# Kernel tuning notes

Measured on AMD Instinct MI355X. Metric: run time of the kernel, lower is better.

The kernel has to match this reference:

```python
import jax, jax.numpy as jnp
import numpy as np

N = 50000      # nodes
E = 800000     # edges
D_IN = 128
D_H = 128
D_OUT = 40
BN_EPS = 1e-5


def setup_inputs() -> dict:
    key = jax.random.key(0)
    ks = jax.random.split(key, 12)
    x = jax.random.normal(ks[0], (N, D_IN), dtype=jnp.float32)
    edge_index = jax.random.randint(ks[1], (2, E), 0, N, dtype=jnp.int32)
    s = 0.05
    W1 = jax.random.normal(ks[2], (D_IN, D_H), dtype=jnp.float32) * s
    b1 = jnp.zeros((D_H,), jnp.float32)
    W2 = jax.random.normal(ks[3], (D_H, D_H), dtype=jnp.float32) * s
    b2 = jnp.zeros((D_H,), jnp.float32)
    W3 = jax.random.normal(ks[4], (D_H, D_OUT), dtype=jnp.float32) * s
    b3 = jnp.zeros((D_OUT,), jnp.float32)
    # BatchNorm (eval mode: running stats)
    g1 = jnp.ones((D_H,), jnp.float32)
    be1 = jnp.zeros((D_H,), jnp.float32)
    m1 = jax.random.normal(ks[5], (D_H,), dtype=jnp.float32) * 0.1
    v1 = jax.random.uniform(ks[6], (D_H,), dtype=jnp.float32, minval=0.5, maxval=1.5)
    g2 = jnp.ones((D_H,), jnp.float32)
    be2 = jnp.zeros((D_H,), jnp.float32)
    m2 = jax.random.normal(ks[7], (D_H,), dtype=jnp.float32) * 0.1
    v2 = jax.random.uniform(ks[8], (D_H,), dtype=jnp.float32, minval=0.5, maxval=1.5)
    return {"x": x, "edge_index": edge_index,
            "W1": W1, "b1": b1, "W2": W2, "b2": b2, "W3": W3, "b3": b3,
            "g1": g1, "be1": be1, "m1": m1, "v1": v1,
            "g2": g2, "be2": be2, "m2": m2, "v2": v2}


def gcn_conv(x, W, b, src, dst):
    # PyG GCNConv: h = x W; A_hat = D^-1/2 (A + I) D^-1/2; out = A_hat h + b
    h = x @ W                                   # [N, d_out]
    deg = jnp.zeros((N,), h.dtype).at[dst].add(1.0) + 1.0   # degrees incl. self loop
    dis = jax.lax.rsqrt(deg)                    # deg^-1/2
    norm = dis[src] * dis[dst]                  # [E]
    msg = h[src] * norm[:, None]                # [E, d_out] gather + scale
    agg = jax.ops.segment_sum(msg, dst, num_segments=N)     # scatter-add
    agg = agg + h * (1.0 / deg)[:, None]        # self-loop term: dis_i*dis_i = 1/deg_i
    return agg + b


def bn_eval(x, gamma, beta, mean, var):
    return (x - mean) * jax.lax.rsqrt(var + BN_EPS) * gamma + beta


def reference(x, edge_index, W1, b1, W2, b2, W3, b3,
              g1, be1, m1, v1, g2, be2, m2, v2):
    src, dst = edge_index[0], edge_index[1]
    h = jax.nn.relu(bn_eval(gcn_conv(x, W1, b1, src, dst), g1, be1, m1, v1))
    h = jax.nn.relu(bn_eval(gcn_conv(h, W2, b2, src, dst), g2, be2, m2, v2))
    h = gcn_conv(h, W3, b3, src, dst)
    return jax.nn.log_softmax(h, axis=-1)
```

## Files before the change

### kernel.cpp

```cpp
#include <hip/hip_runtime.h>
#include <math.h>

#define BN_EPS 1e-5f

typedef __attribute__((ext_vector_type(8))) short bf16x8;
typedef __attribute__((ext_vector_type(4))) float f32x4;

__device__ inline unsigned f2bf(float f) {
  union { float f; unsigned u; } v; v.f = f;
  unsigned r = v.u + 0x7FFF + ((v.u >> 16) & 1);
  return r >> 16;
}

__device__ inline void acc8n(float* a, uint4 v) {
  a[0] += __uint_as_float(v.x << 16);
  a[1] += __uint_as_float(v.x & 0xffff0000u);
  a[2] += __uint_as_float(v.y << 16);
  a[3] += __uint_as_float(v.y & 0xffff0000u);
  a[4] += __uint_as_float(v.z << 16);
  a[5] += __uint_as_float(v.z & 0xffff0000u);
  a[6] += __uint_as_float(v.w << 16);
  a[7] += __uint_as_float(v.w & 0xffff0000u);
}

__device__ inline void acc4n(float* a, uint2 v) {
  a[0] += __uint_as_float(v.x << 16);
  a[1] += __uint_as_float(v.x & 0xffff0000u);
  a[2] += __uint_as_float(v.y << 16);
  a[3] += __uint_as_float(v.y & 0xffff0000u);
}


__global__ void k_zero(uint4* __restrict__ deg, int n16, uint4* __restrict__ flags) {
  int i = blockIdx.x * blockDim.x + threadIdx.x;
  if (i < n16) deg[i] = make_uint4(0, 0, 0, 0);
  if (i < 16) flags[i] = make_uint4(0, 0, 0, 0);
}


__global__ __launch_bounds__(256) void k_count_prep(
    const int* __restrict__ ei, int E, int* __restrict__ deg, int* __restrict__ posw,
    const float* __restrict__ W1, const float* __restrict__ W2,
    const float* __restrict__ W3,
    const float* __restrict__ g1, const float* __restrict__ be1,
    const float* __restrict__ m1, const float* __restrict__ v1,
    const float* __restrict__ g2, const float* __restrict__ be2,
    const float* __restrict__ m2, const float* __restrict__ v2,
    const float* __restrict__ b1, const float* __restrict__ b2,
    const float* __restrict__ b3,
    ushort* __restrict__ WT1, ushort* __restrict__ WT2, ushort* __restrict__ WT3,
    float* __restrict__ sc1, float* __restrict__ sh1,
    float* __restrict__ sc2, float* __restrict__ sh2,
    float* __restrict__ b3pad) {
  int b = blockIdx.x;
  int tid = threadIdx.x;
  if (b < 64) {
    int k = b * 2 + (tid >> 7);
    int n = tid & 127;
    WT1[n * 128 + k] = (ushort)f2bf(W1[k * 128 + n]);
    WT2[n * 128 + k] = (ushort)f2bf(W2[k * 128 + n]);
    WT3[n * 128 + k] = (n < 40) ? (ushort)f2bf(W3[k * 40 + n]) : (ushort)0;
    if (k == 0) {
      float s1 = g1[n] * rsqrtf(v1[n] + BN_EPS);
      sc1[n] = s1; sh1[n] = be1[n] + (b1[n] - m1[n]) * s1;
      float s2 = g2[n] * rsqrtf(v2[n] + BN_EPS);
      sc2[n] = s2; sh2[n] = be2[n] + (b2[n] - m2[n]) * s2;
    } else if (k == 1 && n < 64) {
      b3pad[n] = (n < 40) ? b3[n] : 0.f;
    }
    return;
  }
  int e = (b - 64) * 256 + tid;
  if (e < E) posw[e] = atomicAdd(&deg[ei[E + e]], 1);
}

__global__ void k_scan(const int* __restrict__ deg, int* __restrict__ rowstart,
                       float* __restrict__ dis, int* __restrict__ flags,
                       int n, int E) {
  __shared__ int s[1024];
  __shared__ int spre;
  const int b = blockIdx.x;
  const int tid = threadIdx.x;
  int i = b * 1024 + tid;
  int v = (i < n) ? deg[i] : 0;
  if (i < n) dis[i] = rsqrtf((float)(v + 1));
  s[tid] = v;
  __syncthreads();
  for (int off = 1; off < 1024; off <<= 1) {
    int t = (tid >= off) ? s[tid - off] : 0;
    __syncthreads();
    s[tid] += t;
    __syncthreads();
  }
  if (tid == 0) {
    spre = 0;
    atomicExch(&flags[b], s[1023] + 1);
  }
  __syncthreads();
  if (tid < b) {
    int v2;
    do { v2 = atomicAdd(&flags[tid], 0); } while (v2 == 0);
    atomicAdd(&spre, v2 - 1);
  }
  __syncthreads();
  int pre = spre;
  if (i < n) rowstart[i] = pre + s[tid] - v;
  if (b == 0 && tid == 0) rowstart[n] = E;
}


template <bool F32A, bool FILL>
__global__ __launch_bounds__(256) void k_gemm_bf16(const void* __restrict__ Ap,
                                                   const ushort* __restrict__ WT,
                                                   ushort* __restrict__ C,
                                                   const float* __restrict__ dis,
                                                   int nrows, int NC, int gemmBlocks,
                                                   const int* __restrict__ ei,
                                                   const int* __restrict__ rowstart,
                                                   const int* __restrict__ posw,
                                                   unsigned* __restrict__ slot, int E) {
  if (FILL && (int)blockIdx.x >= gemmBlocks) {
    int e = ((int)blockIdx.x - gemmBlocks) * 256 + threadIdx.x;
    if (e < E) slot[rowstart[ei[E + e]] + posw[e]] = (unsigned)ei[e];
    return;
  }
  __shared__ ushort As[64][80];
  __shared__ ushort Bs[128][80];
  const int tid  = threadIdx.x;
  const int lane = tid & 63;
  const int wid  = tid >> 6;
  const int wr   = wid >> 1, wc = wid & 1;
  const int row0 = blockIdx.x * 64;
  f32x4 acc[2][4] = {};

  const int mrow = lane & 15;
  const int kg   = (lane >> 4) * 8;

  for (int k0 = 0; k0 < 128; k0 += 64) {
    __syncthreads();
    for (int i = tid; i < 512; i += 256) {
      int r = i >> 3, c = (i & 7) * 8;
      uint4 w = make_uint4(0, 0, 0, 0);
      if (row0 + r < nrows) {
        if (F32A) {
          const float* A = (const float*)Ap;
          float4 v0 = *(const float4*)(A + (size_t)(row0 + r) * 128 + k0 + c);
          float4 v1 = *(const float4*)(A + (size_t)(row0 + r) * 128 + k0 + c + 4);
          w.x = f2bf(v0.x) | (f2bf(v0.y) << 16);
          w.y = f2bf(v0.z) | (f2bf(v0.w) << 16);
          w.z = f2bf(v1.x) | (f2bf(v1.y) << 16);
          w.w = f2bf(v1.z) | (f2bf(v1.w) << 16);
        } else {
          const ushort* A = (const ushort*)Ap;
          w = *(const uint4*)(A + (size_t)(row0 + r) * 128 + k0 + c);
        }
      }
      *(uint4*)(&As[r][c]) = w;
    }
    for (int i = tid; i < 1024; i += 256) {
      int r = i >> 3, c = (i & 7) * 8;
      *(uint4*)(&Bs[r][c]) = *(const uint4*)(WT + r * 128 + k0 + c);
    }
    __syncthreads();

#pragma unroll
    for (int ks = 0; ks < 2; ks++) {
      bf16x8 a[2], b[4];
#pragma unroll
      for (int f = 0; f < 2; f++)
        a[f] = *(const bf16x8*)(&As[wr * 32 + f * 16 + mrow][ks * 32 + kg]);
#pragma unroll
      for (int f = 0; f < 4; f++)
        b[f] = *(const bf16x8*)(&Bs[wc * 64 + f * 16 + mrow][ks * 32 + kg]);
#pragma unroll
      for (int fm = 0; fm < 2; fm++)
#pragma unroll
        for (int fn = 0; fn < 4; fn++)
          acc[fm][fn] = __builtin_amdgcn_mfma_f32_16x16x32_bf16(a[fm], b[fn], acc[fm][fn], 0, 0, 0);
    }
  }

  const int rl = (lane >> 4) * 4;
  const int cl = lane & 15;
#pragma unroll
  for (int fm = 0; fm < 2; fm++) {
#pragma unroll
    for (int r = 0; r < 4; r++) {
      int row = row0 + wr * 32 + fm * 16 + rl + r;
      if (row >= nrows) continue;
      float dn = dis[row];
#pragma unroll
      for (int fn = 0; fn < 4; fn++) {
        int col = wc * 64 + fn * 16 + cl;
        if (col < NC) C[(size_t)row * NC + col] = (ushort)f2bf(acc[fm][fn][r] * dn);
      }
    }
  }
}


__global__ __launch_bounds__(256) void k_agg128b(const ushort* __restrict__ h,
                          const int* __restrict__ rowstart,
                          const unsigned* __restrict__ slot,
                          const float* __restrict__ dis,
                          const float* __restrict__ bnsc,
                          const float* __restrict__ bnsh,
                          ushort* __restrict__ out, int nnodes) {
  int node = blockIdx.x * 4 + threadIdx.y;
  if (node >= nnodes) return;
  int lane = threadIdx.x;
  int eg = lane >> 4, cl = lane & 15, c0 = cl * 8;
  int s = rowstart[node], e = rowstart[node + 1];
  int deg = e - s;
  unsigned mys = 0;
  if (lane < deg) mys = slot[s + lane];
  float a[8] = {0.f, 0.f, 0.f, 0.f, 0.f, 0.f, 0.f, 0.f};
  int nb = deg < 64 ? deg : 64;
  int i = eg;
  for (; i + 12 < nb; i += 16) {
    int s0 = __shfl((int)mys, i);
    int s1 = __shfl((int)mys, i + 4);
    int s2 = __shfl((int)mys, i + 8);
    int s3 = __shfl((int)mys, i + 12);
    uint4 h0 = *(const uint4*)(h + (size_t)s0 * 128 + c0);
    uint4 h1 = *(const uint4*)(h + (size_t)s1 * 128 + c0);
    uint4 h2 = *(const uint4*)(h + (size_t)s2 * 128 + c0);
    uint4 h3 = *(const uint4*)(h + (size_t)s3 * 128 + c0);
    acc8n(a, h0); acc8n(a, h1); acc8n(a, h2); acc8n(a, h3);
  }
  for (; i + 4 < nb; i += 8) {
    int s0 = __shfl((int)mys, i);
    int s1 = __shfl((int)mys, i + 4);
    uint4 h0 = *(const uint4*)(h + (size_t)s0 * 128 + c0);
    uint4 h1 = *(const uint4*)(h + (size_t)s1 * 128 + c0);
    acc8n(a, h0); acc8n(a, h1);
  }
  if (i < nb) {
    int s0 = __shfl((int)mys, i);
    uint4 h0 = *(const uint4*)(h + (size_t)s0 * 128 + c0);
    acc8n(a, h0);
  }
  for (int j = s + 64 + eg; j < e; j += 4) {
    uint4 h0 = *(const uint4*)(h + (size_t)slot[j] * 128 + c0);
    acc8n(a, h0);
  }
#pragma unroll
  for (int j = 0; j < 8; j++) {
    a[j] += __shfl_xor(a[j], 16);
    a[j] += __shfl_xor(a[j], 32);
  }
  if (eg == 0) {
    uint4 hv = *(const uint4*)(h + (size_t)node * 128 + c0);
    acc8n(a, hv);
    float dn = dis[node];
    float4 sc0 = *(const float4*)(bnsc + c0), sc1 = *(const float4*)(bnsc + c0 + 4);
    float4 sh0 = *(const float4*)(bnsh + c0), sh1 = *(const float4*)(bnsh + c0 + 4);
    float o0 = fmaxf(fmaf(a[0] * dn, sc0.x, sh0.x), 0.f);
    float o1 = fmaxf(fmaf(a[1] * dn, sc0.y, sh0.y), 0.f);
    float o2 = fmaxf(fmaf(a[2] * dn, sc0.z, sh0.z), 0.f);
    float o3 = fmaxf(fmaf(a[3] * dn, sc0.w, sh0.w), 0.f);
    float o4 = fmaxf(fmaf(a[4] * dn, sc1.x, sh1.x), 0.f);
    float o5 = fmaxf(fmaf(a[5] * dn, sc1.y, sh1.y), 0.f);
    float o6 = fmaxf(fmaf(a[6] * dn, sc1.z, sh1.z), 0.f);
    float o7 = fmaxf(fmaf(a[7] * dn, sc1.w, sh1.w), 0.f);
    uint4 w;
    w.x = f2bf(o0) | (f2bf(o1) << 16);
    w.y = f2bf(o2) | (f2bf(o3) << 16);
    w.z = f2bf(o4) | (f2bf(o5) << 16);
    w.w = f2bf(o6) | (f2bf(o7) << 16);
    *(uint4*)(out + (size_t)node * 128 + c0) = w;
  }
}


__global__ __launch_bounds__(256) void k_agg40_lsm(const ushort* __restrict__ h,
                            const int* __restrict__ rowstart,
                            const unsigned* __restrict__ slot,
                            const float* __restrict__ dis,
                            const float* __restrict__ b3pad,
                            float* __restrict__ out, int nnodes) {
  int node = blockIdx.x * 4 + threadIdx.y;
  if (node >= nnodes) return;
  int lane = threadIdx.x;
  int eg = lane >> 4, cl = lane & 15, c0 = cl * 4;
  bool act = cl < 10;
  int s = rowstart[node], e = rowstart[node + 1];
  int deg = e - s;
  unsigned mys = 0;
  if (lane < deg) mys = slot[s + lane];
  float a[4] = {0.f, 0.f, 0.f, 0.f};
  int nb = deg < 64 ? deg : 64;
  int i = eg;
  for (; i + 12 < nb; i += 16) {
    int s0 = __shfl((int)mys, i);
    int s1 = __shfl((int)mys, i + 4);
    int s2 = __shfl((int)mys, i + 8);
    int s3 = __shfl((int)mys, i + 12);
    if (act) {
      uint2 h0 = *(const uint2*)(h + (size_t)s0 * 40 + c0);
      uint2 h1 = *(const uint2*)(h + (size_t)s1 * 40 + c0);
      uint2 h2 = *(const uint2*)(h + (size_t)s2 * 40 + c0);
      uint2 h3 = *(const uint2*)(h + (size_t)s3 * 40 + c0);
      acc4n(a, h0); acc4n(a, h1); acc4n(a, h2); acc4n(a, h3);
    }
  }
  for (; i + 4 < nb; i += 8) {
    int s0 = __shfl((int)mys, i);
    int s1 = __shfl((int)mys, i + 4);
    if (act) {
      uint2 h0 = *(const uint2*)(h + (size_t)s0 * 40 + c0);
      uint2 h1 = *(const uint2*)(h + (size_t)s1 * 40 + c0);
      acc4n(a, h0); acc4n(a, h1);
    }
  }
  if (i < nb) {
    int s0 = __shfl((int)mys, i);
    if (act) acc4n(a, *(const uint2*)(h + (size_t)s0 * 40 + c0));
  }
  for (int j = s + 64 + eg; j < e; j += 4) {
    unsigned sj = slot[j];
    if (act) acc4n(a, *(const uint2*)(h + (size_t)sj * 40 + c0));
  }
#pragma unroll
  for (int j = 0; j < 4; j++) {
    a[j] += __shfl_xor(a[j], 16);
    a[j] += __shfl_xor(a[j], 32);
  }
  if (act) {
    acc4n(a, *(const uint2*)(h + (size_t)node * 40 + c0));
    float dn = dis[node];
    float4 bb = *(const float4*)(b3pad + c0);
    a[0] = fmaf(a[0], dn, bb.x);
    a[1] = fmaf(a[1], dn, bb.y);
    a[2] = fmaf(a[2], dn, bb.z);
    a[3] = fmaf(a[3], dn, bb.w);
  }
  float m = act ? fmaxf(fmaxf(a[0], a[1]), fmaxf(a[2], a[3])) : -INFINITY;
#pragma unroll
  for (int off = 1; off < 16; off <<= 1) m = fmaxf(m, __shfl_xor(m, off));
  float ss = act ? (expf(a[0] - m) + expf(a[1] - m) + expf(a[2] - m) + expf(a[3] - m)) : 0.f;
#pragma unroll
  for (int off = 1; off < 16; off <<= 1) ss += __shfl_xor(ss, off);
  float lse = m + logf(ss);
  if (eg == 0 && act) {
    *(float4*)(out + (size_t)node * 40 + c0) =
        make_float4(a[0] - lse, a[1] - lse, a[2] - lse, a[3] - lse);
  }
}


extern "C" void kernel_launch(void* const* d_in, const int* in_sizes, int n_in,
                              void* d_out, int out_size, void* d_ws, size_t ws_size,
                              hipStream_t stream) {
  const float* x   = (const float*)d_in[0];
  const int*   ei  = (const int*)d_in[1];
  const float* W1  = (const float*)d_in[2];
  const float* b1  = (const float*)d_in[3];
  const float* W2  = (const float*)d_in[4];
  const float* b2  = (const float*)d_in[5];
  const float* W3  = (const float*)d_in[6];
  const float* b3  = (const float*)d_in[7];
  const float* g1  = (const float*)d_in[8];
  const float* be1 = (const float*)d_in[9];
  const float* m1  = (const float*)d_in[10];
  const float* v1  = (const float*)d_in[11];
  const float* g2  = (const float*)d_in[12];
  const float* be2 = (const float*)d_in[13];
  const float* m2  = (const float*)d_in[14];
  const float* v2  = (const float*)d_in[15];

  const int N   = in_sizes[0] / 128;
  const int E   = in_sizes[1] / 2;

  float* outp = (float*)d_out;

  char* ws = (char*)d_ws;
  size_t off = 0;
  auto alloc = [&](size_t bytes) -> char* {
    char* p = ws + off;
    off = (off + bytes + 255) & ~(size_t)255;
    return p;
  };
  const int deg16 = (N + 3) / 4;
  int*      deg      = (int*)alloc((size_t)deg16 * 16);
  int*      flags    = (int*)alloc(64 * 4);
  int*      posw     = (int*)alloc((size_t)E * 4);
  int*      rowstart = (int*)alloc((size_t)(N + 1) * 4);
  float*    dis      = (float*)alloc((size_t)N * 4);
  unsigned* slot     = (unsigned*)alloc((size_t)E * 4);
  float*    sc1      = (float*)alloc(128 * 4);
  float*    sh1      = (float*)alloc(128 * 4);
  float*    sc2      = (float*)alloc(128 * 4);
  float*    sh2      = (float*)alloc(128 * 4);
  float*    b3pad    = (float*)alloc(64 * 4);
  ushort*   WT1      = (ushort*)alloc(128 * 128 * 2);
  ushort*   WT2      = (ushort*)alloc(128 * 128 * 2);
  ushort*   WT3      = (ushort*)alloc(128 * 128 * 2);
  ushort*   bufA     = (ushort*)alloc((size_t)N * 128 * 2);
  ushort*   bufB     = (ushort*)alloc((size_t)N * 128 * 2);
  ushort*   bufC     = (ushort*)alloc((size_t)N * 40 * 2);
  (void)ws_size;

  const int T = 256;
  const int chunks = (N + 1023) / 1024;
  const int cBlocks = (E + 255) / 256;

  k_zero<<<(deg16 + T - 1) / T, T, 0, stream>>>((uint4*)deg, deg16, (uint4*)flags);
  k_count_prep<<<64 + cBlocks, 256, 0, stream>>>(
      ei, E, deg, posw, W1, W2, W3, g1, be1, m1, v1, g2, be2, m2, v2,
      b1, b2, b3, WT1, WT2, WT3, sc1, sh1, sc2, sh2, b3pad);
  k_scan<<<chunks, 1024, 0, stream>>>(deg, rowstart, dis, flags, N, E);

  const int quads = (N + 3) / 4;
  dim3 aggBlk(64, 4);
  const int gBlocks = (N + 63) / 64;

  k_gemm_bf16<true, true><<<gBlocks + cBlocks, 256, 0, stream>>>(
      x, WT1, bufB, dis, N, 128, gBlocks, ei, rowstart, posw, slot, E);
  k_agg128b<<<quads, aggBlk, 0, stream>>>(bufB, rowstart, slot, dis, sc1, sh1, bufA, N);

  k_gemm_bf16<false, false><<<gBlocks, 256, 0, stream>>>(
      bufA, WT2, bufB, dis, N, 128, gBlocks, nullptr, nullptr, nullptr, nullptr, 0);
  k_agg128b<<<quads, aggBlk, 0, stream>>>(bufB, rowstart, slot, dis, sc2, sh2, bufA, N);

  k_gemm_bf16<false, false><<<gBlocks, 256, 0, stream>>>(
      bufA, WT3, bufC, dis, N, 40, gBlocks, nullptr, nullptr, nullptr, nullptr, 0);
  k_agg40_lsm<<<quads, aggBlk, 0, stream>>>(bufC, rowstart, slot, dis, b3pad, outp, N);
}
```

Measured before the change: 184.4 us.

## Add dedicated 40-column GEMM and pack two nodes per wave in final aggregation

Result: faster. 170.4 us (-7.6%).

```diff
diff --git a/kernel.cpp b/kernel.cpp
--- a/kernel.cpp
+++ b/kernel.cpp
@@ -114,7 +114,7 @@
                                                    const ushort* __restrict__ WT,
                                                    ushort* __restrict__ C,
                                                    const float* __restrict__ dis,
-                                                   int nrows, int NC, int gemmBlocks,
+                                                   int nrows, int gemmBlocks,
                                                    const int* __restrict__ ei,
                                                    const int* __restrict__ rowstart,
                                                    const int* __restrict__ posw,
@@ -192,8 +192,67 @@
 #pragma unroll
       for (int fn = 0; fn < 4; fn++) {
         int col = wc * 64 + fn * 16 + cl;
-        if (col < NC) C[(size_t)row * NC + col] = (ushort)f2bf(acc[fm][fn][r] * dn);
+        C[(size_t)row * 128 + col] = (ushort)f2bf(acc[fm][fn][r] * dn);
       }
+    }
+  }
+}
+
+
+__global__ __launch_bounds__(256) void k_gemm40(const ushort* __restrict__ A,
+                                                const ushort* __restrict__ WT,
+                                                ushort* __restrict__ C,
+                                                const float* __restrict__ dis,
+                                                int nrows) {
+  __shared__ ushort As[64][80];
+  __shared__ ushort Bs[48][80];
+  const int tid  = threadIdx.x;
+  const int lane = tid & 63;
+  const int wid  = tid >> 6;
+  const int row0 = blockIdx.x * 64;
+  f32x4 acc[3] = {};
+
+  const int mrow = lane & 15;
+  const int kg   = (lane >> 4) * 8;
+
+  for (int k0 = 0; k0 < 128; k0 += 64) {
+    __syncthreads();
+    for (int i = tid; i < 512; i += 256) {
+      int r = i >> 3, c = (i & 7) * 8;
+      uint4 w = make_uint4(0, 0, 0, 0);
+      if (row0 + r < nrows) w = *(const uint4*)(A + (size_t)(row0 + r) * 128 + k0 + c);
+      *(uint4*)(&As[r][c]) = w;
+    }
+    for (int i = tid; i < 384; i += 256) {
+      int r = i >> 3, c = (i & 7) * 8;
+      *(uint4*)(&Bs[r][c]) = *(const uint4*)(WT + r * 128 + k0 + c);
+    }
+    __syncthreads();
+
+#pragma unroll
+    for (int ks = 0; ks < 2; ks++) {
+      bf16x8 a = *(const bf16x8*)(&As[wid * 16 + mrow][ks * 32 + kg]);
+      bf16x8 b[3];
+#pragma unroll
+      for (int f = 0; f < 3; f++)
+        b[f] = *(const bf16x8*)(&Bs[f * 16 + mrow][ks * 32 + kg]);
+#pragma unroll
+      for (int f = 0; f < 3; f++)
+        acc[f] = __builtin_amdgcn_mfma_f32_16x16x32_bf16(a, b[f], acc[f], 0, 0, 0);
+    }
+  }
+
+  const int rl = (lane >> 4) * 4;
+  const int cl = lane & 15;
+#pragma unroll
+  for (int r = 0; r < 4; r++) {
+    int row = row0 + wid * 16 + rl + r;
+    if (row >= nrows) continue;
+    float dn = dis[row];
+#pragma unroll
+    for (int f = 0; f < 3; f++) {
+      int col = f * 16 + cl;
+      if (col < 40) C[(size_t)row * 40 + col] = (ushort)f2bf(acc[f][r] * dn);
     }
   }
 }
@@ -279,23 +338,24 @@
                             const float* __restrict__ dis,
                             const float* __restrict__ b3pad,
                             float* __restrict__ out, int nnodes) {
-  int node = blockIdx.x * 4 + threadIdx.y;
+  int lane = threadIdx.x;
+  int node = blockIdx.x * 8 + threadIdx.y * 2 + (lane >> 5);
   if (node >= nnodes) return;
-  int lane = threadIdx.x;
-  int eg = lane >> 4, cl = lane & 15, c0 = cl * 4;
+  int eg = (lane >> 4) & 1, cl = lane & 15, c0 = cl * 4;
   bool act = cl < 10;
   int s = rowstart[node], e = rowstart[node + 1];
   int deg = e - s;
+  int l32 = lane & 31;
   unsigned mys = 0;
-  if (lane < deg) mys = slot[s + lane];
+  if (l32 < deg) mys = slot[s + l32];
   float a[4] = {0.f, 0.f, 0.f, 0.f};
-  int nb = deg < 64 ? deg : 64;
+  int nb = deg < 32 ? deg : 32;
   int i = eg;
-  for (; i + 12 < nb; i += 16) {
-    int s0 = __shfl((int)mys, i);
-    int s1 = __shfl((int)mys, i + 4);
-    int s2 = __shfl((int)mys, i + 8);
-    int s3 = __shfl((int)mys, i + 12);
+  for (; i + 6 < nb; i += 8) {
+    int s0 = __shfl((int)mys, i, 32);
+    int s1 = __shfl((int)mys, i + 2, 32);
+    int s2 = __shfl((int)mys, i + 4, 32);
+    int s3 = __shfl((int)mys, i + 6, 32);
     if (act) {
       uint2 h0 = *(const uint2*)(h + (size_t)s0 * 40 + c0);
       uint2 h1 = *(const uint2*)(h + (size_t)s1 * 40 + c0);
@@ -304,28 +364,16 @@
       acc4n(a, h0); acc4n(a, h1); acc4n(a, h2); acc4n(a, h3);
     }
   }
-  for (; i + 4 < nb; i += 8) {
-    int s0 = __shfl((int)mys, i);
-    int s1 = __shfl((int)mys, i + 4);
-    if (act) {
-      uint2 h0 = *(const uint2*)(h + (size_t)s0 * 40 + c0);
-      uint2 h1 = *(const uint2*)(h + (size_t)s1 * 40 + c0);
-      acc4n(a, h0); acc4n(a, h1);
-    }
-  }
-  if (i < nb) {
-    int s0 = __shfl((int)mys, i);
+  for (; i < nb; i += 2) {
+    int s0 = __shfl((int)mys, i, 32);
     if (act) acc4n(a, *(const uint2*)(h + (size_t)s0 * 40 + c0));
   }
-  for (int j = s + 64 + eg; j < e; j += 4) {
+  for (int j = s + 32 + eg; j < e; j += 2) {
     unsigned sj = slot[j];
     if (act) acc4n(a, *(const uint2*)(h + (size_t)sj * 40 + c0));
   }
 #pragma unroll
-  for (int j = 0; j < 4; j++) {
-    a[j] += __shfl_xor(a[j], 16);
-    a[j] += __shfl_xor(a[j], 32);
-  }
+  for (int j = 0; j < 4; j++) a[j] += __shfl_xor(a[j], 16);
   if (act) {
     acc4n(a, *(const uint2*)(h + (size_t)node * 40 + c0));
     float dn = dis[node];
@@ -416,14 +464,13 @@
   const int gBlocks = (N + 63) / 64;
 
   k_gemm_bf16<true, true><<<gBlocks + cBlocks, 256, 0, stream>>>(
-      x, WT1, bufB, dis, N, 128, gBlocks, ei, rowstart, posw, slot, E);
+      x, WT1, bufB, dis, N, gBlocks, ei, rowstart, posw, slot, E);
   k_agg128b<<<quads, aggBlk, 0, stream>>>(bufB, rowstart, slot, dis, sc1, sh1, bufA, N);
 
   k_gemm_bf16<false, false><<<gBlocks, 256, 0, stream>>>(
-      bufA, WT2, bufB, dis, N, 128, gBlocks, nullptr, nullptr, nullptr, nullptr, 0);
+      bufA, WT2, bufB, dis, N, gBlocks, nullptr, nullptr, nullptr, nullptr, 0);
   k_agg128b<<<quads, aggBlk, 0, stream>>>(bufB, rowstart, slot, dis, sc2, sh2, bufA, N);
 
-  k_gemm_bf16<false, false><<<gBlocks, 256, 0, stream>>>(
-      bufA, WT3, bufC, dis, N, 40, gBlocks, nullptr, nullptr, nullptr, nullptr, 0);
-  k_agg40_lsm<<<quads, aggBlk, 0, stream>>>(bufC, rowstart, slot, dis, b3pad, outp, N);
-}
+  k_gemm40<<<gBlocks, 256, 0, stream>>>(bufA, WT3, bufC, dis, N);
+  k_agg40_lsm<<<(N + 7) / 8, aggBlk, 0, stream>>>(bufC, rowstart, slot, dis, b3pad, outp, N);
+}
```
